# Kernel tuning notes

Measured on AMD Instinct MI355X. Metric: run time of the kernel, lower is better.

The kernel has to match this reference:

```python
import jax, jax.numpy as jnp
from jax import lax
import numpy as np

KSIZE = 3      # patch size for correlation
RATE = 2       # downsample rate; raw kernel = 2*RATE
FUSE_K = 3     # diagonal fuse kernel
SCALE = 10.0   # softmax_scale
DOWN_RATE = 8  # mask downsample
EPS = 1e-4
DN = ('NCHW', 'OIHW', 'NCHW')


def same_pad(x, k, s):
    H, W = x.shape[-2], x.shape[-1]
    oh, ow = -(-H // s), -(-W // s)
    ph = max(0, (oh - 1) * s + k - H)
    pw = max(0, (ow - 1) * s + k - W)
    pt, pl = ph // 2, pw // 2
    pad = [(0, 0)] * (x.ndim - 2) + [(pt, ph - pt), (pl, pw - pl)]
    return jnp.pad(x, pad)


def extract_patches(x, k, s):
    # x: [B,C,H,W] -> [B, L, C, k, k], matching torch unfold ordering
    B, C, H, W = x.shape
    oh, ow = -(-H // s), -(-W // s)
    xp = same_pad(x, k, s)
    cols = [xp[:, :, i:i + oh * s:s, j:j + ow * s:s] for i in range(k) for j in range(k)]
    p = jnp.stack(cols, axis=2).reshape(B, C, k, k, oh * ow)
    return p.transpose(0, 4, 1, 2, 3)


def conv1x1(x, w, b):  # x: [L,C,kh,kw], w: [D,C], b: [D]
    return jnp.einsum('lcij,dc->ldij', x, w) + b[None, :, None, None]


def setup_inputs():
    key = jax.random.key(0)
    B, C, H, W = 4, 128, 96, 96
    D = C // 8
    ks = jax.random.split(key, 6)
    f = jax.random.normal(ks[0], (B, C, H, W), jnp.float32)
    b = jax.random.normal(ks[1], (B, C, H, W), jnp.float32)
    mask = jnp.ones((B, 1, 4 * H, 4 * W), jnp.float32)
    mask = mask.at[:, :, 120:264, 120:264].set(0.0)  # rectangular hole
    s = 0.05
    wq = jax.random.normal(ks[2], (D, C), jnp.float32) * s
    bq = jnp.zeros((D,), jnp.float32)
    wk = jax.random.normal(ks[3], (D, C), jnp.float32) * s
    bk = jnp.zeros((D,), jnp.float32)
    wv = jax.random.normal(ks[4], (C, C), jnp.float32) * s
    bv = jnp.zeros((C,), jnp.float32)
    beta_2 = jnp.asarray(1.0, jnp.float32)
    return dict(f=f, b=b, mask=mask, wq=wq, bq=bq, wk=wk, bk=bk, wv=wv, bv=bv,
                beta_2=beta_2)


def reference(f, b, mask, wq, bq, wk, bk, wv, bv, beta_2):
    B, C, H, W = f.shape
    raw_w = extract_patches(b, 2 * RATE, RATE)          # [B, L, C, 4, 4]
    f_ds = f[:, :, ::RATE, ::RATE]                      # nearest 1/RATE
    b_ds = b[:, :, ::RATE, ::RATE]
    h, w_ = f_ds.shape[2], f_ds.shape[3]
    L = h * w_
    w_p = extract_patches(b_ds, KSIZE, 1)               # [B, L, C, 3, 3]
    fw_p = extract_patches(f_ds, KSIZE, 1)              # [B, L, C, 3, 3]
    m_ds = mask[:, :, ::DOWN_RATE, ::DOWN_RATE]
    m = extract_patches(m_ds, KSIZE, 1)[0]              # [L, 1, 3, 3] (batch 0, as in original)
    mm = lax.stop_gradient(
        (jnp.mean(m, axis=(1, 2, 3)) == 0.0).astype(f.dtype)).reshape(L, 1, 1)
    eye = jnp.eye(FUSE_K, dtype=f.dtype).reshape(1, 1, FUSE_K, FUSE_K)

    def one(fi_p, wi_p, xi, raw_wi):
        # intra-patch pixel attention (9x9 per patch)
        q = conv1x1(fi_p, wq, bq).reshape(L, -1, 9).transpose(0, 2, 1)   # [L,9,D]
        k_ = conv1x1(wi_p, wk, bk).reshape(L, -1, 9)                     # [L,D,9]
        sim = jnp.einsum('lnd,ldm->lnm', q, k_) * m.reshape(L, 1, 9)
        attn = jax.nn.softmax(sim, axis=-1)
        v = conv1x1(fi_p, wv, bv).reshape(L, C, 9)
        final = jnp.einsum('lcn,lmn->lcm', v, attn).reshape(L, C, KSIZE, KSIZE)
        final = beta_2 * fi_p * m + (1.0 - m) * final
        # normalize patch kernels
        norm = jnp.maximum(jnp.sqrt(jnp.sum(final * final, axis=(1, 2, 3), keepdims=True)), EPS)
        wn = final / norm                                                 # [L,C,3,3]
        # patch-correlation: conv with data-dependent kernels
        yi = lax.conv_general_dilated(same_pad(xi[None], KSIZE, 1), wn,
                                      (1, 1), 'VALID', dimension_numbers=DN)  # [1,L,h,w]
        # fuse: two diagonal-propagation convolutions
        y2 = yi.reshape(1, 1, L, L)
        y2 = lax.conv_general_dilated(y2, eye, (1, 1), ((1, 1), (1, 1)), dimension_numbers=DN)
        y2 = y2.reshape(h, w_, h, w_).transpose(1, 0, 3, 2).reshape(1, 1, L, L)
        y2 = lax.conv_general_dilated(y2, eye, (1, 1), ((1, 1), (1, 1)), dimension_numbers=DN)
        y2 = y2.reshape(w_, h, w_, h).transpose(1, 0, 3, 2)               # [h,w,h,w]
        yi = y2.reshape(L, h, w_) * mm
        yi = jax.nn.softmax(yi * SCALE, axis=0) * mm
        # conv_transpose2d(stride=RATE, padding=1) via lhs-dilated conv
        wt = jnp.flip(raw_wi, (-2, -1)).transpose(1, 0, 2, 3)             # [C,L,4,4]
        out = lax.conv_general_dilated(yi[None], wt, (1, 1), ((2, 2), (2, 2)),
                                       lhs_dilation=(RATE, RATE),
                                       dimension_numbers=DN) / 4.0
        return out[0]                                                     # [C,H,W]

    return jax.vmap(one)(fw_p, w_p, f_ds, raw_w)
```

## Files before the change

### kernel.cpp

```cpp
#include <hip/hip_runtime.h>
#include <math.h>


constexpr int B_ = 4, C_ = 128, D_ = 16;
constexpr int FH = 96, FW = 96;
constexpr int Hh = 48, Wd = 48;
constexpr int L_ = Hh * Wd;
constexpr int NEED_CAP = 384, HOLE_CAP = 320;
constexpr int KC = C_ * 9;
constexpr int QKV_ROWS = 208;
constexpr int NQK = NEED_CAP * 9;
constexpr float SCALE_ = 10.0f;
constexpr float EPS_ = 1e-4f;

typedef __attribute__((ext_vector_type(8))) short bf16x8;
typedef __attribute__((ext_vector_type(4))) float f32x4;
typedef __attribute__((ext_vector_type(4))) short s16x4;
typedef __attribute__((ext_vector_type(2))) unsigned short u16x2;

static __device__ __forceinline__ f32x4 mfma16(bf16x8 a, bf16x8 b, f32x4 c) {
  return __builtin_amdgcn_mfma_f32_16x16x32_bf16(a, b, c, 0, 0, 0);
}
static __device__ __forceinline__ unsigned short bf16_rne(float f) {
  unsigned u = __builtin_bit_cast(unsigned, f);
  unsigned r = (u + 0x7FFFu + ((u >> 16) & 1u)) >> 16;
  return (unsigned short)r;
}
static __device__ __forceinline__ float bf16f(unsigned short h) {
  unsigned u = ((unsigned)h) << 16;
  return __builtin_bit_cast(float, u);
}
static __device__ __forceinline__ void split2(float v, unsigned short& hi, unsigned short& lo) {
  hi = bf16_rne(v);
  lo = bf16_rne(v - bf16f(hi));
}

constexpr size_t A256(size_t v) { return (v + 255) & ~size_t(255); }
constexpr size_t OFF_META  = 0;
constexpr size_t OFF_MP    = A256(OFF_META + 64 * 4);
constexpr size_t OFF_MM    = A256(OFF_MP + (size_t)L_ * 9 * 4);
constexpr size_t OFF_ROWL  = A256(OFF_MM + (size_t)L_ * 4);
constexpr size_t OFF_NLIST = A256(OFF_ROWL + (size_t)L_ * 4);
constexpr size_t OFF_HLIST = A256(OFF_NLIST + (size_t)NEED_CAP * 4);
constexpr size_t OFF_WQVH  = A256(OFF_HLIST + (size_t)HOLE_CAP * 4);
constexpr size_t OFF_WQVL  = A256(OFF_WQVH + (size_t)192 * 128 * 2);
constexpr size_t OFF_WKH   = A256(OFF_WQVL + (size_t)192 * 128 * 2);
constexpr size_t OFF_WKL   = A256(OFF_WKH + (size_t)64 * 128 * 2);
constexpr size_t OFF_FDSH  = A256(OFF_WKL + (size_t)64 * 128 * 2);
constexpr size_t OFF_FDSL  = A256(OFF_FDSH + (size_t)B_ * L_ * C_ * 2);
constexpr size_t OFF_BDSH  = A256(OFF_FDSL + (size_t)B_ * L_ * C_ * 2);
constexpr size_t OFF_BDSL  = A256(OFF_BDSH + (size_t)B_ * L_ * C_ * 2);
constexpr size_t OFF_QKV   = A256(OFF_BDSL + (size_t)B_ * L_ * C_ * 2);
constexpr size_t OFF_SF    = OFF_QKV;
constexpr size_t OFF_WNH   = A256(OFF_QKV + (size_t)B_ * QKV_ROWS * NQK * 4);
constexpr size_t OFF_WNL   = A256(OFF_WNH + (size_t)B_ * NEED_CAP * KC * 2);
constexpr size_t OFF_SRAW  = A256(OFF_WNL + (size_t)B_ * NEED_CAP * KC * 2);
constexpr size_t OFF_PHT   = OFF_SRAW;
constexpr size_t OFF_PLT   = OFF_SRAW + (size_t)B_ * L_ * HOLE_CAP * 2;
constexpr size_t OFF_RW3H  = A256(OFF_SRAW + (size_t)B_ * NEED_CAP * L_ * 4);
constexpr size_t OFF_RW3L  = A256(OFF_RW3H + (size_t)B_ * 4 * C_ * 1280 * 2);
constexpr size_t OFF_OUTS  = A256(OFF_RW3L + (size_t)B_ * 4 * C_ * 1280 * 2);

__global__ __launch_bounds__(256) void gla_wpack(const float* __restrict__ wq, const float* __restrict__ wk,
                                                 const float* __restrict__ wv, char* __restrict__ ws)
{
  int i = blockIdx.x * 256 + threadIdx.x;
  unsigned short* qvh = (unsigned short*)(ws + OFF_WQVH);
  unsigned short* qvl = (unsigned short*)(ws + OFF_WQVL);
  unsigned short* kh  = (unsigned short*)(ws + OFF_WKH);
  unsigned short* kl  = (unsigned short*)(ws + OFF_WKL);
  if (i < 192 * 128) {
    int row = i >> 7, c = i & 127;
    float v = 0.f;
    if (row < 16) v = wq[row * C_ + c];
    else if (row < 144) v = wv[(row - 16) * C_ + c];
    unsigned short hi, lo; split2(v, hi, lo);
    qvh[i] = hi; qvl[i] = lo;
  } else if (i < 256 * 128) {
    int j = i - 192 * 128;
    int row = j >> 7, c = j & 127;
    float v = (row < 16) ? wk[row * C_ + c] : 0.f;
    unsigned short hi, lo; split2(v, hi, lo);
    kh[j] = hi; kl[j] = lo;
  }
}

__global__ __launch_bounds__(256) void gla_maskA(const float* __restrict__ mask, char* __restrict__ ws)
{
  int l = blockIdx.x * 256 + threadIdx.x;
  if (l >= L_) return;
  float* m_p = (float*)(ws + OFF_MP);
  int* mmi = (int*)(ws + OFF_MM);
  int y = l / Wd, x = l % Wd;
  bool all0 = true;
  #pragma unroll
  for (int dy = 0; dy < 3; dy++)
    #pragma unroll
    for (int dx = 0; dx < 3; dx++) {
      int sy = y + dy - 1, sx = x + dx - 1;
      float v = ((unsigned)sy < (unsigned)Hh && (unsigned)sx < (unsigned)Wd)
                ? mask[(size_t)(8 * sy) * 384 + 8 * sx] : 0.f;
      m_p[l * 9 + dy * 3 + dx] = v;
      if (v != 0.f) all0 = false;
    }
  mmi[l] = all0 ? 1 : 0;
}

__global__ __launch_bounds__(256) void gla_scan(char* __restrict__ ws)
{
  const int* mmi = (const int*)(ws + OFF_MM);
  int* row_l = (int*)(ws + OFF_ROWL);
  int* nlist = (int*)(ws + OFF_NLIST);
  int* hlist = (int*)(ws + OFF_HLIST);
  int* meta  = (int*)(ws + OFF_META);
  __shared__ int ns1[L_], nraw[L_];
  __shared__ int sN[256], sH[256];
  const int t = threadIdx.x;
  for (int l = t; l < L_; l += 256) { ns1[l] = 0; nraw[l] = 0; }
  __syncthreads();
  for (int l = t; l < L_; l += 256) {
    if (mmi[l]) {
      int i = l / Wd, j = l % Wd;
      int p2 = j * Hh + i;
      for (int k2 = -1; k2 <= 1; k2++) {
        int p2k = p2 + k2;
        if (p2k >= 0 && p2k < L_) {
          int j2 = p2k / Hh, i2 = p2k % Hh;
          ns1[i2 * Wd + j2] = 1;
        }
      }
    }
  }
  __syncthreads();
  for (int l = t; l < L_; l += 256) {
    if (ns1[l]) {
      for (int k1 = -1; k1 <= 1; k1++) {
        int l3 = l + k1;
        if (l3 >= 0 && l3 < L_) nraw[l3] = 1;
      }
    }
  }
  __syncthreads();
  int cN = 0, cH = 0;
  for (int q = 0; q < 9; q++) {
    int l = t * 9 + q;
    if (nraw[l]) cN++;
    if (mmi[l]) cH++;
  }
  sN[t] = cN; sH[t] = cH;
  __syncthreads();
  for (int off = 1; off < 256; off <<= 1) {
    int vN = (t >= off) ? sN[t - off] : 0;
    int vH = (t >= off) ? sH[t - off] : 0;
    __syncthreads();
    sN[t] += vN; sH[t] += vH;
    __syncthreads();
  }
  int bN = sN[t] - cN, bH = sH[t] - cH;
  for (int q = 0; q < 9; q++) {
    int l = t * 9 + q;
    int rl = -1;
    if (nraw[l]) { if (bN < NEED_CAP) { nlist[bN] = l; rl = bN; } bN++; }
    row_l[l] = rl;
    if (mmi[l]) { if (bH < HOLE_CAP) { hlist[bH] = l; } bH++; }
  }
  if (t == 255) {
    meta[0] = sN[255] < NEED_CAP ? sN[255] : NEED_CAP;
    meta[1] = sH[255] < HOLE_CAP ? sH[255] : HOLE_CAP;
  }
}

__global__ __launch_bounds__(256) void gla_splitfb(const float* __restrict__ f, const float* __restrict__ b,
                                                   char* __restrict__ ws)
{
  const int y = blockIdx.x, ib = blockIdx.y, z = blockIdx.z;
  const float* src = z ? b : f;
  unsigned short* dsth = (unsigned short*)(ws + (z ? OFF_BDSH : OFF_FDSH));
  unsigned short* dstl = (unsigned short*)(ws + (z ? OFF_BDSL : OFF_FDSL));
  __shared__ float tile[48][130];
  const int t = threadIdx.x;
  for (int idx = t; idx < 48 * C_; idx += 256) {
    int x = idx % 48, c = idx / 48;
    tile[x][c] = src[(((size_t)ib * C_ + c) * FH + 2 * y) * FW + 2 * x];
  }
  __syncthreads();
  for (int i = 0; i < 12; i++) {
    int p = t + i * 256;
    int c2 = p & 63, x = p >> 6;
    float v0 = tile[x][c2 * 2], v1 = tile[x][c2 * 2 + 1];
    unsigned short h0, l0, h1, l1;
    split2(v0, h0, l0);
    split2(v1, h1, l1);
    size_t o = ((size_t)ib * L_ + (size_t)y * Wd + x) * C_ + c2 * 2;
    *(u16x2*)&dsth[o] = u16x2{h0, h1};
    *(u16x2*)&dstl[o] = u16x2{l0, l1};
  }
}

__global__ __launch_bounds__(256) void gla_qkv(const float* __restrict__ bq, const float* __restrict__ bk,
                                               const float* __restrict__ bv, char* __restrict__ ws)
{
  const int* meta = (const int*)(ws + OFF_META);
  const int need = meta[0];
  int orig = blockIdx.x;
  int wg = (orig & 7) * 54 + (orig >> 3);
  bool isK = wg >= 324;
  int ib, mt, nt;
  if (!isK) { ib = wg / 81; int r2 = wg % 81; mt = r2 / 27; nt = r2 % 27; }
  else { int q2 = wg - 324; ib = q2 / 27; mt = 0; nt = q2 % 27; }
  const int m0 = mt * 64, n0 = nt * 128;
  const unsigned short* Ahg = (const unsigned short*)(ws + (isK ? OFF_WKH : OFF_WQVH));
  const unsigned short* Alg = (const unsigned short*)(ws + (isK ? OFF_WKL : OFF_WQVL));
  const unsigned short* Bhg = (const unsigned short*)(ws + (isK ? OFF_BDSH : OFF_FDSH)) + (size_t)ib * L_ * C_;
  const unsigned short* Blg = (const unsigned short*)(ws + (isK ? OFF_BDSL : OFF_FDSL)) + (size_t)ib * L_ * C_;
  const int* nlist = (const int*)(ws + OFF_NLIST);
  float* QKV = (float*)(ws + OFF_QKV) + (size_t)ib * QKV_ROWS * NQK;

  __shared__ short Ah[64][40], Al[64][40], Bh[128][40], Bl[128][40];
  const int tid = threadIdx.x;
  const int lane = tid & 63, w = tid >> 6;
  const int fr = lane & 15, kq = (lane >> 4) * 8;
  const int arow = tid & 63, aj = tid >> 6;
  const int bcol = tid & 127, bj = tid >> 7;

  const int col = n0 + bcol;
  const int r = col / 9, tap = col % 9;
  bool valid = (r < need);
  size_t bpos = 0;
  if (valid) {
    int l = nlist[r];
    int y = l / Wd, x = l % Wd;
    int sy = y + tap / 3 - 1, sx = x + tap % 3 - 1;
    valid = ((unsigned)sy < (unsigned)Hh) && ((unsigned)sx < (unsigned)Wd);
    if (valid) bpos = (size_t)(sy * Wd + sx) * C_;
  }

  f32x4 acc[4][2];
  #pragma unroll
  for (int mi = 0; mi < 4; mi++)
    #pragma unroll
    for (int ni = 0; ni < 2; ni++)
      #pragma unroll
      for (int q = 0; q < 4; q++) acc[mi][ni][q] = 0.f;

  const bf16x8 zz = {0, 0, 0, 0, 0, 0, 0, 0};
  bf16x8 rah, ral, rbh0, rbh1, rbl0, rbl1;
  auto load_step = [&](int s) {
    int k0 = s * 32;
    size_t aoff = (size_t)(m0 + arow) * 128 + k0 + aj * 8;
    rah = *(const bf16x8*)&Ahg[aoff];
    ral = *(const bf16x8*)&Alg[aoff];
    if (valid) {
      size_t boff = bpos + k0 + bj * 16;
      rbh0 = *(const bf16x8*)&Bhg[boff];
      rbh1 = *(const bf16x8*)&Bhg[boff + 8];
      rbl0 = *(const bf16x8*)&Blg[boff];
      rbl1 = *(const bf16x8*)&Blg[boff + 8];
    } else {
      rbh0 = zz; rbh1 = zz; rbl0 = zz; rbl1 = zz;
    }
  };

  load_step(0);
  for (int s = 0; s < 4; s++) {
    __syncthreads();
    *(bf16x8*)&Ah[arow][aj * 8] = rah;
    *(bf16x8*)&Al[arow][aj * 8] = ral;
    *(bf16x8*)&Bh[bcol][bj * 16] = rbh0;
    *(bf16x8*)&Bh[bcol][bj * 16 + 8] = rbh1;
    *(bf16x8*)&Bl[bcol][bj * 16] = rbl0;
    *(bf16x8*)&Bl[bcol][bj * 16 + 8] = rbl1;
    __syncthreads();
    if (s < 3) load_step(s + 1);
    bf16x8 a_h[4], a_l[4], b_h[2], b_l[2];
    #pragma unroll
    for (int mi = 0; mi < 4; mi++) {
      a_h[mi] = *(const bf16x8*)&Ah[mi * 16 + fr][kq];
      a_l[mi] = *(const bf16x8*)&Al[mi * 16 + fr][kq];
    }
    #pragma unroll
    for (int ni = 0; ni < 2; ni++) {
      b_h[ni] = *(const bf16x8*)&Bh[w * 32 + ni * 16 + fr][kq];
      b_l[ni] = *(const bf16x8*)&Bl[w * 32 + ni * 16 + fr][kq];
    }
    #pragma unroll
    for (int mi = 0; mi < 4; mi++)
      #pragma unroll
      for (int ni = 0; ni < 2; ni++) {
        acc[mi][ni] = mfma16(a_h[mi], b_h[ni], acc[mi][ni]);
        acc[mi][ni] = mfma16(a_h[mi], b_l[ni], acc[mi][ni]);
        acc[mi][ni] = mfma16(a_l[mi], b_h[ni], acc[mi][ni]);
      }
  }
  #pragma unroll
  for (int mi = 0; mi < 4; mi++)
    #pragma unroll
    for (int ni = 0; ni < 2; ni++) {
      int rowb = m0 + mi * 16 + (lane >> 4) * 4;
      int colg = n0 + w * 32 + ni * 16 + fr;
      #pragma unroll
      for (int q = 0; q < 4; q++) {
        int row = rowb + q;
        float v = acc[mi][ni][q];
        if (!isK) {
          float bias = row < 16 ? bq[row] : (row < 144 ? bv[row - 16] : 0.f);
          QKV[(size_t)row * NQK + colg] = v + bias;
        } else if (row < 16) {
          QKV[(size_t)(192 + row) * NQK + colg] = v + bk[row];
        }
      }
    }
}

__global__ __launch_bounds__(128) void gla_patch2(const float* __restrict__ beta2p, char* __restrict__ ws)
{
  const int* meta = (const int*)(ws + OFF_META);
  int r = blockIdx.x;
  if (r >= meta[0]) return;
  int ib = blockIdx.y;
  const int* nlist = (const int*)(ws + OFF_NLIST);
  const float* m_p = (const float*)(ws + OFF_MP);
  const float* QKV = (const float*)(ws + OFF_QKV) + (size_t)ib * QKV_ROWS * NQK;
  const unsigned short* fdsh = (const unsigned short*)(ws + OFF_FDSH) + (size_t)ib * L_ * C_;
  const unsigned short* fdsl = (const unsigned short*)(ws + OFF_FDSL) + (size_t)ib * L_ * C_;
  unsigned short* wnh = (unsigned short*)(ws + OFF_WNH) + ((size_t)ib * NEED_CAP + r) * KC;
  unsigned short* wnl = (unsigned short*)(ws + OFF_WNL) + ((size_t)ib * NEED_CAP + r) * KC;

  __shared__ float qs[144], ks[144], att[81], mps[9], red[128];
  const int t = threadIdx.x;
  const int l = nlist[r];
  const int y = l / Wd, x = l % Wd;
  const int colb = r * 9;

  if (t < 9) mps[t] = m_p[l * 9 + t];
  for (int o = t; o < 288; o += 128) {
    if (o < 144) {
      int n = o / 16, d = o % 16;
      qs[o] = QKV[(size_t)d * NQK + colb + n];
    } else {
      int o2 = o - 144;
      int d = o2 / 9, m = o2 % 9;
      ks[o2] = QKV[(size_t)(192 + d) * NQK + colb + m];
    }
  }
  __syncthreads();
  if (t < 81) {
    int n = t / 9, m = t % 9;
    float s = 0.f;
    #pragma unroll
    for (int d = 0; d < 16; d++) s += qs[n * 16 + d] * ks[d * 9 + m];
    att[t] = s * mps[m];
  }
  __syncthreads();
  if (t < 9) {
    float mx = -1e30f;
    for (int m = 0; m < 9; m++) mx = fmaxf(mx, att[t * 9 + m]);
    float e[9], sm = 0.f;
    for (int m = 0; m < 9; m++) { e[m] = expf(att[t * 9 + m] - mx); sm += e[m]; }
    float inv = 1.f / sm;
    for (int m = 0; m < 9; m++) att[t * 9 + m] = e[m] * inv;
  }
  __syncthreads();
  const int c = t;
  float vn[9], fi[9];
  #pragma unroll
  for (int n = 0; n < 9; n++) vn[n] = QKV[(size_t)(16 + c) * NQK + colb + n];
  #pragma unroll
  for (int m = 0; m < 9; m++) {
    int sy = y + m / 3 - 1, sx = x + m % 3 - 1;
    float v = 0.f;
    if ((unsigned)sy < (unsigned)Hh && (unsigned)sx < (unsigned)Wd) {
      size_t o = (size_t)(sy * Wd + sx) * C_ + c;
      v = bf16f(fdsh[o]) + bf16f(fdsl[o]);
    }
    fi[m] = v;
  }
  float beta2 = beta2p[0];
  float fm[9];
  #pragma unroll
  for (int m = 0; m < 9; m++) {
    float s = 0.f;
    #pragma unroll
    for (int n = 0; n < 9; n++) s += vn[n] * att[m * 9 + n];
    float mp = mps[m];
    fm[m] = beta2 * fi[m] * mp + (1.f - mp) * s;
  }
  float ss = 0.f;
  #pragma unroll
  for (int m = 0; m < 9; m++) ss += fm[m] * fm[m];
  red[t] = ss;
  __syncthreads();
  for (int off = 64; off > 0; off >>= 1) {
    if (t < off) red[t] += red[t + off];
    __syncthreads();
  }
  float inv = 1.f / fmaxf(sqrtf(red[0]), EPS_);
  #pragma unroll
  for (int m = 0; m < 9; m++) {
    unsigned short hi, lo;
    split2(fm[m] * inv, hi, lo);
    wnh[m * C_ + c] = hi;
    wnl[m * C_ + c] = lo;
  }
}

__global__ __launch_bounds__(256) void gla_corr(char* __restrict__ ws)
{
  int orig = blockIdx.x;
  int wg = (orig & 7) * 54 + (orig >> 3);
  int xt = wg % 18;
  int rt = (wg / 18) % 6;
  int ib = wg / 108;
  const int r0 = rt * 64, x0 = xt * 128;

  const unsigned short* Ahg = (const unsigned short*)(ws + OFF_WNH) + (size_t)ib * NEED_CAP * KC;
  const unsigned short* Alg = (const unsigned short*)(ws + OFF_WNL) + (size_t)ib * NEED_CAP * KC;
  const unsigned short* fh = (const unsigned short*)(ws + OFF_FDSH) + (size_t)ib * L_ * C_;
  const unsigned short* fl = (const unsigned short*)(ws + OFF_FDSL) + (size_t)ib * L_ * C_;
  float* S = (float*)(ws + OFF_SRAW) + (size_t)ib * NEED_CAP * L_;

  __shared__ short Ah[64][40], Al[64][40], Bh[128][40], Bl[128][40];
  const int tid = threadIdx.x;
  const int lane = tid & 63, w = tid >> 6;
  const int fr = lane & 15, kq = (lane >> 4) * 8;
  const int arow = tid & 63, aj = tid >> 6;
  const int bcol = tid & 127, bj = tid >> 7;
  const int xg = x0 + bcol;
  const int aa = xg / Wd, bb = xg % Wd;

  f32x4 acc[4][2];
  #pragma unroll
  for (int mi = 0; mi < 4; mi++)
    #pragma unroll
    for (int ni = 0; ni < 2; ni++)
      #pragma unroll
      for (int q = 0; q < 4; q++) acc[mi][ni][q] = 0.f;

  const bf16x8 zz = {0, 0, 0, 0, 0, 0, 0, 0};
  bf16x8 rah, ral, rbh0, rbh1, rbl0, rbl1;

  auto load_step = [&](int s) {
    int tap = s >> 2, kc = s & 3;
    size_t aoff = (size_t)(r0 + arow) * KC + tap * 128 + kc * 32 + aj * 8;
    rah = *(const bf16x8*)&Ahg[aoff];
    ral = *(const bf16x8*)&Alg[aoff];
    int dyv = tap / 3, dxv = tap - 3 * dyv;
    int sy = aa + dyv - 1, sx = bb + dxv - 1;
    if (((unsigned)sy < (unsigned)Hh) & ((unsigned)sx < (unsigned)Wd)) {
      size_t bpos = (size_t)(sy * Wd + sx) * C_ + kc * 32 + bj * 16;
      rbh0 = *(const bf16x8*)&fh[bpos];
      rbh1 = *(const bf16x8*)&fh[bpos + 8];
      rbl0 = *(const bf16x8*)&fl[bpos];
      rbl1 = *(const bf16x8*)&fl[bpos + 8];
    } else {
      rbh0 = zz; rbh1 = zz; rbl0 = zz; rbl1 = zz;
    }
  };

  load_step(0);
  for (int s = 0; s < 36; s++) {
    __syncthreads();
    *(bf16x8*)&Ah[arow][aj * 8] = rah;
    *(bf16x8*)&Al[arow][aj * 8] = ral;
    *(bf16x8*)&Bh[bcol][bj * 16] = rbh0;
    *(bf16x8*)&Bh[bcol][bj * 16 + 8] = rbh1;
    *(bf16x8*)&Bl[bcol][bj * 16] = rbl0;
    *(bf16x8*)&Bl[bcol][bj * 16 + 8] = rbl1;
    __syncthreads();
    if (s < 35) load_step(s + 1);
    bf16x8 a_h[4], a_l[4], b_h[2], b_l[2];
    #pragma unroll
    for (int mi = 0; mi < 4; mi++) {
      a_h[mi] = *(const bf16x8*)&Ah[mi * 16 + fr][kq];
      a_l[mi] = *(const bf16x8*)&Al[mi * 16 + fr][kq];
    }
    #pragma unroll
    for (int ni = 0; ni < 2; ni++) {
      b_h[ni] = *(const bf16x8*)&Bh[w * 32 + ni * 16 + fr][kq];
      b_l[ni] = *(const bf16x8*)&Bl[w * 32 + ni * 16 + fr][kq];
    }
    #pragma unroll
    for (int mi = 0; mi < 4; mi++)
      #pragma unroll
      for (int ni = 0; ni < 2; ni++) {
        acc[mi][ni] = mfma16(a_h[mi], b_h[ni], acc[mi][ni]);
        acc[mi][ni] = mfma16(a_h[mi], b_l[ni], acc[mi][ni]);
        acc[mi][ni] = mfma16(a_l[mi], b_h[ni], acc[mi][ni]);
      }
  }
  #pragma unroll
  for (int mi = 0; mi < 4; mi++)
    #pragma unroll
    for (int ni = 0; ni < 2; ni++) {
      int row0 = r0 + mi * 16 + (lane >> 4) * 4;
      int col = x0 + w * 32 + ni * 16 + fr;
      #pragma unroll
      for (int q = 0; q < 4; q++)
        S[(size_t)(row0 + q) * L_ + col] = acc[mi][ni][q];
    }
}

__global__ __launch_bounds__(256) void gla_fuse(char* __restrict__ ws)
{
  const int* meta = (const int*)(ws + OFF_META);
  int rh = blockIdx.y;
  if (rh >= meta[1]) return;
  int ib = blockIdx.z;
  const int* hlist = (const int*)(ws + OFF_HLIST);
  const int* row_l = (const int*)(ws + OFF_ROWL);
  const float* S = (const float*)(ws + OFF_SRAW) + (size_t)ib * NEED_CAP * L_;
  float* Sf = (float*)(ws + OFF_SF) + ((size_t)ib * HOLE_CAP + rh) * L_;
  int x = blockIdx.x * 256 + threadIdx.x;
  int l = hlist[rh];
  int i = l / Wd, j = l % Wd;
  int a = x / Wd, b = x % Wd;
  int p2 = j * Hh + i, q2 = b * Hh + a;
  float acc = 0.f;
  #pragma unroll
  for (int k2 = -1; k2 <= 1; k2++) {
    int p2k = p2 + k2, q2k = q2 + k2;
    if (p2k < 0 || p2k >= L_ || q2k < 0 || q2k >= L_) continue;
    int j2 = p2k / Hh, i2 = p2k % Hh;
    int b2 = q2k / Hh, a2 = q2k % Hh;
    int l1 = i2 * Wd + j2, x1 = a2 * Wd + b2;
    #pragma unroll
    for (int k1 = -1; k1 <= 1; k1++) {
      int l3 = l1 + k1, x3 = x1 + k1;
      if (l3 < 0 || l3 >= L_ || x3 < 0 || x3 >= L_) continue;
      int r = row_l[l3];
      if (r >= 0) acc += S[(size_t)r * L_ + x3];
    }
  }
  Sf[x] = acc;
}

__global__ __launch_bounds__(256) void gla_softmax(char* __restrict__ ws)
{
  const int* meta = (const int*)(ws + OFF_META);
  const int hc = meta[1];
  const int ib = blockIdx.y;
  const int t = threadIdx.x;
  const int xl = t & 63, g = t >> 6;
  const int x0 = blockIdx.x * 64;
  const float* Sf = (const float*)(ws + OFF_SF) + (size_t)ib * HOLE_CAP * L_;
  unsigned short* Ph = (unsigned short*)(ws + OFF_PHT) + (size_t)ib * L_ * HOLE_CAP;
  unsigned short* Pl = (unsigned short*)(ws + OFF_PLT) + (size_t)ib * L_ * HOLE_CAP;
  __shared__ float red[4][64];
  __shared__ float smx[64], sinv[64];
  __shared__ short Th[64][72], Tl[64][72];
  const int x = x0 + xl;
  float mx = 0.f;
  for (int rh = g; rh < hc; rh += 4) mx = fmaxf(mx, SCALE_ * Sf[(size_t)rh * L_ + x]);
  red[g][xl] = mx;
  __syncthreads();
  mx = fmaxf(fmaxf(red[0][xl], red[1][xl]), fmaxf(red[2][xl], red[3][xl]));
  __syncthreads();
  float s = 0.f;
  for (int rh = g; rh < hc; rh += 4) s += expf(SCALE_ * Sf[(size_t)rh * L_ + x] - mx);
  red[g][xl] = s;
  __syncthreads();
  float den = (float)(L_ - hc) * expf(-mx) + red[0][xl] + red[1][xl] + red[2][xl] + red[3][xl];
  if (g == 0) { smx[xl] = mx; sinv[xl] = 1.f / den; }
  __syncthreads();
  for (int rh0 = 0; rh0 < HOLE_CAP; rh0 += 64) {
    for (int i = 0; i < 16; i++) {
      int idx = t + i * 256;
      int xl2 = idx & 63, rr = idx >> 6;
      int rh = rh0 + rr;
      float e = 0.f;
      if (rh < hc) e = expf(SCALE_ * Sf[(size_t)rh * L_ + x0 + xl2] - smx[xl2]) * sinv[xl2];
      unsigned short hi, lo;
      split2(e, hi, lo);
      Th[xl2][rr] = (short)hi;
      Tl[xl2][rr] = (short)lo;
    }
    __syncthreads();
    for (int i = 0; i < 4; i++) {
      int q = t + i * 256;
      int rq = q & 15, xl2 = q >> 4;
      size_t dst = (size_t)(x0 + xl2) * HOLE_CAP + rh0 + rq * 4;
      *(s16x4*)&Ph[dst] = *(const s16x4*)&Th[xl2][rq * 4];
      *(s16x4*)&Pl[dst] = *(const s16x4*)&Tl[xl2][rq * 4];
    }
    __syncthreads();
  }
}

__global__ __launch_bounds__(256) void gla_packRW3(const float* __restrict__ b, char* __restrict__ ws)
{
  int idx = blockIdx.x * 256 + threadIdx.x;
  const int tot = B_ * 4 * C_ * 1280;
  if (idx >= tot) return;
  const int* meta = (const int*)(ws + OFF_META);
  const int* hlist = (const int*)(ws + OFF_HLIST);
  unsigned short* RH = (unsigned short*)(ws + OFF_RW3H);
  unsigned short* RL = (unsigned short*)(ws + OFF_RW3L);
  int kk = idx % 1280;
  int c = (idx / 1280) & 127;
  int par = (idx / (1280 * 128)) & 3;
  int ib = idx / (1280 * 128 * 4);
  int tap = kk / 320, rh = kk % 320;
  int dy = tap >> 1, dx = tap & 1;
  int pY = par >> 1, pX = par & 1;
  float v = 0.f;
  if (rh < meta[1]) {
    int l = hlist[rh];
    int yy = l / Wd, xx = l % Wd;
    int ty = 2 * dy + ((pY + 1) & 1);
    int tx = 2 * dx + ((pX + 1) & 1);
    int sy = 2 * yy - 1 + ty, sx = 2 * xx - 1 + tx;
    if ((unsigned)sy < (unsigned)FH && (unsigned)sx < (unsigned)FW)
      v = b[(((size_t)ib * C_ + c) * FH + sy) * FW + sx];
  }
  unsigned short hi, lo;
  split2(v, hi, lo);
  RH[idx] = hi;
  RL[idx] = lo;
}

__global__ __launch_bounds__(256) void gla_out(char* __restrict__ ws)
{
  const int* meta = (const int*)(ws + OFF_META);
  const int rsteps = (meta[1] + 31) >> 5;
  const int nsteps = 4 * rsteps;
  int orig = blockIdx.x;
  int wg = (orig & 7) * 144 + (orig >> 3);
  int nt = wg % 36;
  int rest = wg / 36;
  int mt = rest & 1;
  int par = (rest >> 1) & 3;
  int ib = rest >> 3;
  const int m0 = mt * 64, n0 = nt * 64;
  const int pY = par >> 1, pX = par & 1;

  const unsigned short* Ahg = (const unsigned short*)(ws + OFF_RW3H) + ((size_t)(ib * 4 + par) * C_) * 1280;
  const unsigned short* Alg = (const unsigned short*)(ws + OFF_RW3L) + ((size_t)(ib * 4 + par) * C_) * 1280;
  const unsigned short* Ph = (const unsigned short*)(ws + OFF_PHT) + (size_t)ib * L_ * HOLE_CAP;
  const unsigned short* Pl = (const unsigned short*)(ws + OFF_PLT) + (size_t)ib * L_ * HOLE_CAP;
  float* OUTS = (float*)(ws + OFF_OUTS) + (size_t)(ib * 4 + par) * C_ * L_;

  __shared__ short Ah[64][40], Al[64][40], Bh[64][40], Bl[64][40];
  const int tid = threadIdx.x;
  const int lane = tid & 63, w = tid >> 6;
  const int fr = lane & 15, kq = (lane >> 4) * 8;
  const int arow = tid & 63, aj = tid >> 6;
  const int bcol = tid & 63, bj = tid >> 6;

  const int colg = n0 + bcol;
  const int Yh = colg / 48, Xh = colg % 48;
  size_t bpos[4];
  bool bval[4];
  #pragma unroll
  for (int j = 0; j < 4; j++) {
    int dy = j >> 1, dx = j & 1;
    int ay = Yh + pY - dy, bx = Xh + pX - dx;
    bval[j] = ((unsigned)ay < 48u) && ((unsigned)bx < 48u);
    bpos[j] = bval[j] ? (size_t)(ay * 48 + bx) * HOLE_CAP : 0;
  }

  f32x4 acc[4];
  #pragma unroll
  for (int mi = 0; mi < 4; mi++)
    #pragma unroll
    for (int q = 0; q < 4; q++) acc[mi][q] = 0.f;

  const bf16x8 zz = {0, 0, 0, 0, 0, 0, 0, 0};
  bf16x8 rah, ral, rbh, rbl;
  auto load_step = [&](int s) {
    int tap = s / rsteps;
    int kr = (s - tap * rsteps) * 32;
    size_t aoff = (size_t)(m0 + arow) * 1280 + tap * 320 + kr + aj * 8;
    rah = *(const bf16x8*)&Ahg[aoff];
    ral = *(const bf16x8*)&Alg[aoff];
    if (bval[tap]) {
      size_t boff = bpos[tap] + kr + bj * 8;
      rbh = *(const bf16x8*)&Ph[boff];
      rbl = *(const bf16x8*)&Pl[boff];
    } else {
      rbh = zz; rbl = zz;
    }
  };

  load_step(0);
  for (int s = 0; s < nsteps; s++) {
    __syncthreads();
    *(bf16x8*)&Ah[arow][aj * 8] = rah;
    *(bf16x8*)&Al[arow][aj * 8] = ral;
    *(bf16x8*)&Bh[bcol][bj * 8] = rbh;
    *(bf16x8*)&Bl[bcol][bj * 8] = rbl;
    __syncthreads();
    if (s + 1 < nsteps) load_step(s + 1);
    bf16x8 b_h = *(const bf16x8*)&Bh[w * 16 + fr][kq];
    bf16x8 b_l = *(const bf16x8*)&Bl[w * 16 + fr][kq];
    #pragma unroll
    for (int mi = 0; mi < 4; mi++) {
      bf16x8 a_h = *(const bf16x8*)&Ah[mi * 16 + fr][kq];
      bf16x8 a_l = *(const bf16x8*)&Al[mi * 16 + fr][kq];
      acc[mi] = mfma16(a_h, b_h, acc[mi]);
      acc[mi] = mfma16(a_h, b_l, acc[mi]);
      acc[mi] = mfma16(a_l, b_h, acc[mi]);
    }
  }
  #pragma unroll
  for (int mi = 0; mi < 4; mi++) {
    int c0 = m0 + mi * 16 + (lane >> 4) * 4;
    int colpos = n0 + w * 16 + fr;
    #pragma unroll
    for (int q = 0; q < 4; q++)
      OUTS[(size_t)(c0 + q) * L_ + colpos] = 0.25f * acc[mi][q];
  }
}

__global__ __launch_bounds__(256) void gla_inter(float* __restrict__ out, const char* __restrict__ ws)
{
  int idx = blockIdx.x * 256 + threadIdx.x;
  if (idx >= B_ * C_ * FH * (FW / 2)) return;
  const float* OUTS = (const float*)(ws + OFF_OUTS);
  int Xh = idx % 48;
  int Y  = (idx / 48) % FH;
  int c  = (idx / (48 * FH)) % C_;
  int ib = idx / (48 * FH * C_);
  int pY = Y & 1, Yh = Y >> 1;
  size_t base = ((size_t)(ib * 4 + pY * 2) * C_ + c) * L_ + Yh * 48 + Xh;
  float2 o2;
  o2.x = OUTS[base];
  o2.y = OUTS[base + (size_t)C_ * L_];
  *(float2*)&out[(((size_t)ib * C_ + c) * FH + Y) * FW + 2 * Xh] = o2;
}

extern "C" void kernel_launch(void* const* d_in, const int* in_sizes, int n_in,
                              void* d_out, int out_size, void* d_ws, size_t ws_size,
                              hipStream_t stream)
{
  (void)in_sizes; (void)n_in; (void)out_size; (void)ws_size;
  const float* f    = (const float*)d_in[0];
  const float* b    = (const float*)d_in[1];
  const float* mask = (const float*)d_in[2];
  const float* wq   = (const float*)d_in[3];
  const float* bq   = (const float*)d_in[4];
  const float* wk   = (const float*)d_in[5];
  const float* bk   = (const float*)d_in[6];
  const float* wv   = (const float*)d_in[7];
  const float* bv   = (const float*)d_in[8];
  const float* bt2  = (const float*)d_in[9];
  float* out = (float*)d_out;
  char* ws = (char*)d_ws;

  hipLaunchKernelGGL(gla_wpack, dim3(128), dim3(256), 0, stream, wq, wk, wv, ws);
  hipLaunchKernelGGL(gla_maskA, dim3(9), dim3(256), 0, stream, mask, ws);
  hipLaunchKernelGGL(gla_scan, dim3(1), dim3(256), 0, stream, ws);
  hipLaunchKernelGGL(gla_splitfb, dim3(Hh, B_, 2), dim3(256), 0, stream, f, b, ws);
  hipLaunchKernelGGL(gla_qkv, dim3(432), dim3(256), 0, stream, bq, bk, bv, ws);
  hipLaunchKernelGGL(gla_patch2, dim3(NEED_CAP, B_), dim3(128), 0, stream, bt2, ws);
  hipLaunchKernelGGL(gla_corr, dim3(432), dim3(256), 0, stream, ws);
  hipLaunchKernelGGL(gla_fuse, dim3(L_ / 256, HOLE_CAP, B_), dim3(256), 0, stream, ws);
  hipLaunchKernelGGL(gla_softmax, dim3(L_ / 64, B_), dim3(256), 0, stream, ws);
  hipLaunchKernelGGL(gla_packRW3, dim3((B_ * 4 * C_ * 1280 + 255) / 256), dim3(256), 0, stream, b, ws);
  hipLaunchKernelGGL(gla_out, dim3(1152), dim3(256), 0, stream, ws);
  hipLaunchKernelGGL(gla_inter, dim3((B_ * C_ * FH * (FW / 2) + 255) / 256), dim3(256), 0, stream, out, ws);
}
```

Measured before the change: 351.7 us.

## Double-buffer LDS in corr/out GEMMs, widen out tile, swizzle fuse grid

```diff
diff --git a/kernel.cpp b/kernel.cpp
--- a/kernel.cpp
+++ b/kernel.cpp
@@ -419,7 +419,7 @@
   const unsigned short* fl = (const unsigned short*)(ws + OFF_FDSL) + (size_t)ib * L_ * C_;
   float* S = (float*)(ws + OFF_SRAW) + (size_t)ib * NEED_CAP * L_;
 
-  __shared__ short Ah[64][40], Al[64][40], Bh[128][40], Bl[128][40];
+  __shared__ short Ah[2][64][40], Al[2][64][40], Bh[2][128][40], Bl[2][128][40];
   const int tid = threadIdx.x;
   const int lane = tid & 63, w = tid >> 6;
   const int fr = lane & 15, kq = (lane >> 4) * 8;
@@ -437,9 +437,11 @@
       for (int q = 0; q < 4; q++) acc[mi][ni][q] = 0.f;
 
   const bf16x8 zz = {0, 0, 0, 0, 0, 0, 0, 0};
-  bf16x8 rah, ral, rbh0, rbh1, rbl0, rbl1;
-
-  auto load_step = [&](int s) {
+  bf16x8 rahA, ralA, rb0A, rb1A, rb2A, rb3A;
+  bf16x8 rahB, ralB, rb0B, rb1B, rb2B, rb3B;
+
+  auto load_step = [&](int s, bf16x8& rah, bf16x8& ral, bf16x8& rbh0, bf16x8& rbh1,
+                       bf16x8& rbl0, bf16x8& rbl1) {
     int tap = s >> 2, kc = s & 3;
     size_t aoff = (size_t)(r0 + arow) * KC + tap * 128 + kc * 32 + aj * 8;
     rah = *(const bf16x8*)&Ahg[aoff];
@@ -456,28 +458,26 @@
       rbh0 = zz; rbh1 = zz; rbl0 = zz; rbl1 = zz;
     }
   };
-
-  load_step(0);
-  for (int s = 0; s < 36; s++) {
-    __syncthreads();
-    *(bf16x8*)&Ah[arow][aj * 8] = rah;
-    *(bf16x8*)&Al[arow][aj * 8] = ral;
-    *(bf16x8*)&Bh[bcol][bj * 16] = rbh0;
-    *(bf16x8*)&Bh[bcol][bj * 16 + 8] = rbh1;
-    *(bf16x8*)&Bl[bcol][bj * 16] = rbl0;
-    *(bf16x8*)&Bl[bcol][bj * 16 + 8] = rbl1;
-    __syncthreads();
-    if (s < 35) load_step(s + 1);
+  auto store_step = [&](int bi, bf16x8 rah, bf16x8 ral, bf16x8 rbh0, bf16x8 rbh1,
+                        bf16x8 rbl0, bf16x8 rbl1) {
+    *(bf16x8*)&Ah[bi][arow][aj * 8] = rah;
+    *(bf16x8*)&Al[bi][arow][aj * 8] = ral;
+    *(bf16x8*)&Bh[bi][bcol][bj * 16] = rbh0;
+    *(bf16x8*)&Bh[bi][bcol][bj * 16 + 8] = rbh1;
+    *(bf16x8*)&Bl[bi][bcol][bj * 16] = rbl0;
+    *(bf16x8*)&Bl[bi][bcol][bj * 16 + 8] = rbl1;
+  };
+  auto compute = [&](int bi) {
     bf16x8 a_h[4], a_l[4], b_h[2], b_l[2];
     #pragma unroll
     for (int mi = 0; mi < 4; mi++) {
-      a_h[mi] = *(const bf16x8*)&Ah[mi * 16 + fr][kq];
-      a_l[mi] = *(const bf16x8*)&Al[mi * 16 + fr][kq];
+      a_h[mi] = *(const bf16x8*)&Ah[bi][mi * 16 + fr][kq];
+      a_l[mi] = *(const bf16x8*)&Al[bi][mi * 16 + fr][kq];
     }
     #pragma unroll
     for (int ni = 0; ni < 2; ni++) {
-      b_h[ni] = *(const bf16x8*)&Bh[w * 32 + ni * 16 + fr][kq];
-      b_l[ni] = *(const bf16x8*)&Bl[w * 32 + ni * 16 + fr][kq];
+      b_h[ni] = *(const bf16x8*)&Bh[bi][w * 32 + ni * 16 + fr][kq];
+      b_l[ni] = *(const bf16x8*)&Bl[bi][w * 32 + ni * 16 + fr][kq];
     }
     #pragma unroll
     for (int mi = 0; mi < 4; mi++)
@@ -487,6 +487,24 @@
         acc[mi][ni] = mfma16(a_h[mi], b_l[ni], acc[mi][ni]);
         acc[mi][ni] = mfma16(a_l[mi], b_h[ni], acc[mi][ni]);
       }
+  };
+
+  const int nsteps = 36;
+  load_step(0, rahA, ralA, rb0A, rb1A, rb2A, rb3A);
+  load_step(1, rahB, ralB, rb0B, rb1B, rb2B, rb3B);
+  store_step(0, rahA, ralA, rb0A, rb1A, rb2A, rb3A);
+  __syncthreads();
+  for (int s = 0; s < nsteps; s += 2) {
+    compute(0);
+    if (s + 2 < nsteps) load_step(s + 2, rahA, ralA, rb0A, rb1A, rb2A, rb3A);
+    store_step(1, rahB, ralB, rb0B, rb1B, rb2B, rb3B);
+    __syncthreads();
+    compute(1);
+    if (s + 3 < nsteps) load_step(s + 3, rahB, ralB, rb0B, rb1B, rb2B, rb3B);
+    if (s + 2 < nsteps) {
+      store_step(0, rahA, ralA, rb0A, rb1A, rb2A, rb3A);
+      __syncthreads();
+    }
   }
   #pragma unroll
   for (int mi = 0; mi < 4; mi++)
@@ -503,14 +521,17 @@
 __global__ __launch_bounds__(256) void gla_fuse(char* __restrict__ ws)
 {
   const int* meta = (const int*)(ws + OFF_META);
-  int rh = blockIdx.y;
+  int orig = blockIdx.x;
+  int wg = (orig & 7) * 1440 + (orig >> 3);
+  int xc = wg % 9;
+  int rh = (wg / 9) % HOLE_CAP;
+  int ib = wg / (9 * HOLE_CAP);
   if (rh >= meta[1]) return;
-  int ib = blockIdx.z;
   const int* hlist = (const int*)(ws + OFF_HLIST);
   const int* row_l = (const int*)(ws + OFF_ROWL);
   const float* S = (const float*)(ws + OFF_SRAW) + (size_t)ib * NEED_CAP * L_;
   float* Sf = (float*)(ws + OFF_SF) + ((size_t)ib * HOLE_CAP + rh) * L_;
-  int x = blockIdx.x * 256 + threadIdx.x;
+  int x = xc * 256 + threadIdx.x;
   int l = hlist[rh];
   int i = l / Wd, j = l % Wd;
   int a = x / Wd, b = x % Wd;
@@ -624,13 +645,12 @@
   const int rsteps = (meta[1] + 31) >> 5;
   const int nsteps = 4 * rsteps;
   int orig = blockIdx.x;
-  int wg = (orig & 7) * 144 + (orig >> 3);
-  int nt = wg % 36;
-  int rest = wg / 36;
-  int mt = rest & 1;
-  int par = (rest >> 1) & 3;
-  int ib = rest >> 3;
-  const int m0 = mt * 64, n0 = nt * 64;
+  int wg = (orig & 7) * 72 + (orig >> 3);
+  int nt = wg % 18;
+  int mt = (wg / 18) % 2;
+  int par = (wg / 36) % 4;
+  int ib = wg / 144;
+  const int m0 = mt * 64, n0 = nt * 128;
   const int pY = par >> 1, pX = par & 1;
 
   const unsigned short* Ahg = (const unsigned short*)(ws + OFF_RW3H) + ((size_t)(ib * 4 + par) * C_) * 1280;
@@ -639,76 +659,104 @@
   const unsigned short* Pl = (const unsigned short*)(ws + OFF_PLT) + (size_t)ib * L_ * HOLE_CAP;
   float* OUTS = (float*)(ws + OFF_OUTS) + (size_t)(ib * 4 + par) * C_ * L_;
 
-  __shared__ short Ah[64][40], Al[64][40], Bh[64][40], Bl[64][40];
+  __shared__ short Ah[2][64][40], Al[2][64][40], Bh[2][128][40], Bl[2][128][40];
   const int tid = threadIdx.x;
   const int lane = tid & 63, w = tid >> 6;
   const int fr = lane & 15, kq = (lane >> 4) * 8;
   const int arow = tid & 63, aj = tid >> 6;
-  const int bcol = tid & 63, bj = tid >> 6;
+  const int bcol = tid & 127, bj = tid >> 7;
 
   const int colg = n0 + bcol;
   const int Yh = colg / 48, Xh = colg % 48;
-  size_t bpos[4];
-  bool bval[4];
-  #pragma unroll
-  for (int j = 0; j < 4; j++) {
-    int dy = j >> 1, dx = j & 1;
-    int ay = Yh + pY - dy, bx = Xh + pX - dx;
-    bval[j] = ((unsigned)ay < 48u) && ((unsigned)bx < 48u);
-    bpos[j] = bval[j] ? (size_t)(ay * 48 + bx) * HOLE_CAP : 0;
-  }
-
-  f32x4 acc[4];
+
+  f32x4 acc[4][2];
   #pragma unroll
   for (int mi = 0; mi < 4; mi++)
     #pragma unroll
-    for (int q = 0; q < 4; q++) acc[mi][q] = 0.f;
+    for (int ni = 0; ni < 2; ni++)
+      #pragma unroll
+      for (int q = 0; q < 4; q++) acc[mi][ni][q] = 0.f;
 
   const bf16x8 zz = {0, 0, 0, 0, 0, 0, 0, 0};
-  bf16x8 rah, ral, rbh, rbl;
-  auto load_step = [&](int s) {
+  bf16x8 rahA, ralA, rb0A, rb1A, rb2A, rb3A;
+  bf16x8 rahB, ralB, rb0B, rb1B, rb2B, rb3B;
+
+  auto load_step = [&](int s, bf16x8& rah, bf16x8& ral, bf16x8& rbh0, bf16x8& rbh1,
+                       bf16x8& rbl0, bf16x8& rbl1) {
     int tap = s / rsteps;
     int kr = (s - tap * rsteps) * 32;
     size_t aoff = (size_t)(m0 + arow) * 1280 + tap * 320 + kr + aj * 8;
     rah = *(const bf16x8*)&Ahg[aoff];
     ral = *(const bf16x8*)&Alg[aoff];
-    if (bval[tap]) {
-      size_t boff = bpos[tap] + kr + bj * 8;
-      rbh = *(const bf16x8*)&Ph[boff];
-      rbl = *(const bf16x8*)&Pl[boff];
+    int ay = Yh + pY - (tap >> 1);
+    int bx = Xh + pX - (tap & 1);
+    if (((unsigned)ay < 48u) & ((unsigned)bx < 48u)) {
+      size_t boff = (size_t)(ay * 48 + bx) * HOLE_CAP + kr + bj * 16;
+      rbh0 = *(const bf16x8*)&Ph[boff];
+      rbh1 = *(const bf16x8*)&Ph[boff + 8];
+      rbl0 = *(const bf16x8*)&Pl[boff];
+      rbl1 = *(const bf16x8*)&Pl[boff + 8];
     } else {
-      rbh = zz; rbl = zz;
+      rbh0 = zz; rbh1 = zz; rbl0 = zz; rbl1 = zz;
     }
   };
-
-  load_step(0);
-  for (int s = 0; s < nsteps; s++) {
+  auto store_step = [&](int bi, bf16x8 rah, bf16x8 ral, bf16x8 rbh0, bf16x8 rbh1,
+                        bf16x8 rbl0, bf16x8 rbl1) {
+    *(bf16x8*)&Ah[bi][arow][aj * 8] = rah;
+    *(bf16x8*)&Al[bi][arow][aj * 8] = ral;
+    *(bf16x8*)&Bh[bi][bcol][bj * 16] = rbh0;
+    *(bf16x8*)&Bh[bi][bcol][bj * 16 + 8] = rbh1;
+    *(bf16x8*)&Bl[bi][bcol][bj * 16] = rbl0;
+    *(bf16x8*)&Bl[bi][bcol][bj * 16 + 8] = rbl1;
+  };
+  auto compute = [&](int bi) {
+    bf16x8 a_h[4], a_l[4], b_h[2], b_l[2];
+    #pragma unroll
+    for (int mi = 0; mi < 4; mi++) {
+      a_h[mi] = *(const bf16x8*)&Ah[bi][mi * 16 + fr][kq];
+      a_l[mi] = *(const bf16x8*)&Al[bi][mi * 16 + fr][kq];
+    }
+    #pragma unroll
+    for (int ni = 0; ni < 2; ni++) {
+      b_h[ni] = *(const bf16x8*)&Bh[bi][w * 32 + ni * 16 + fr][kq];
+      b_l[ni] = *(const bf16x8*)&Bl[bi][w * 32 + ni * 16 + fr][kq];
+    }
+    #pragma unroll
+    for (int mi = 0; mi < 4; mi++)
+      #pragma unroll
+      for (int ni = 0; ni < 2; ni++) {
+        acc[mi][ni] = mfma16(a_h[mi], b_h[ni], acc[mi][ni]);
+        acc[mi][ni] = mfma16(a_h[mi], b_l[ni], acc[mi][ni]);
+        acc[mi][ni] = mfma16(a_l[mi], b_h[ni], acc[mi][ni]);
+      }
+  };
+
+  load_step(0, rahA, ralA, rb0A, rb1A, rb2A, rb3A);
+  load_step(1, rahB, ralB, rb0B, rb1B, rb2B, rb3B);
+  store_step(0, rahA, ralA, rb0A, rb1A, rb2A, rb3A);
+  __syncthreads();
+  for (int s = 0; s < nsteps; s += 2) {
+    compute(0);
+    if (s + 2 < nsteps) load_step(s + 2, rahA, ralA, rb0A, rb1A, rb2A, rb3A);
+    store_step(1, rahB, ralB, rb0B, rb1B, rb2B, rb3B);
     __syncthreads();
-    *(bf16x8*)&Ah[arow][aj * 8] = rah;
-    *(bf16x8*)&Al[arow][aj * 8] = ral;
-    *(bf16x8*)&Bh[bcol][bj * 8] = rbh;
-    *(bf16x8*)&Bl[bcol][bj * 8] = rbl;
-    __syncthreads();
-    if (s + 1 < nsteps) load_step(s + 1);
-    bf16x8 b_h = *(const bf16x8*)&Bh[w * 16 + fr][kq];
-    bf16x8 b_l = *(const bf16x8*)&Bl[w * 16 + fr][kq];
-    #pragma unroll
-    for (int mi = 0; mi < 4; mi++) {
-      bf16x8 a_h = *(const bf16x8*)&Ah[mi * 16 + fr][kq];
-      bf16x8 a_l = *(const bf16x8*)&Al[mi * 16 + fr][kq];
-      acc[mi] = mfma16(a_h, b_h, acc[mi]);
-      acc[mi] = mfma16(a_h, b_l, acc[mi]);
-      acc[mi] = mfma16(a_l, b_h, acc[mi]);
-    }
-  }
-  #pragma unroll
-  for (int mi = 0; mi < 4; mi++) {
-    int c0 = m0 + mi * 16 + (lane >> 4) * 4;
-    int colpos = n0 + w * 16 + fr;
-    #pragma unroll
-    for (int q = 0; q < 4; q++)
-      OUTS[(size_t)(c0 + q) * L_ + colpos] = 0.25f * acc[mi][q];
-  }
+    compute(1);
+    if (s + 3 < nsteps) load_step(s + 3, rahB, ralB, rb0B, rb1B, rb2B, rb3B);
+    if (s + 2 < nsteps) {
+      store_step(0, rahA, ralA, rb0A, rb1A, rb2A, rb3A);
+      __syncthreads();
+    }
+  }
+  #pragma unroll
+  for (int mi = 0; mi < 4; mi++)
+    #pragma unroll
+    for (int ni = 0; ni < 2; ni++) {
+      int c0 = m0 + mi * 16 + (lane >> 4) * 4;
+      int colpos = n0 + w * 32 + ni * 16 + fr;
+      #pragma unroll
+      for (int q = 0; q < 4; q++)
+        OUTS[(size_t)(c0 + q) * L_ + colpos] = 0.25f * acc[mi][ni][q];
+    }
 }
 
 __global__ __launch_bounds__(256) void gla_inter(float* __restrict__ out, const char* __restrict__ ws)
@@ -753,9 +801,9 @@
   hipLaunchKernelGGL(gla_qkv, dim3(432), dim3(256), 0, stream, bq, bk, bv, ws);
   hipLaunchKernelGGL(gla_patch2, dim3(NEED_CAP, B_), dim3(128), 0, stream, bt2, ws);
   hipLaunchKernelGGL(gla_corr, dim3(432), dim3(256), 0, stream, ws);
-  hipLaunchKernelGGL(gla_fuse, dim3(L_ / 256, HOLE_CAP, B_), dim3(256), 0, stream, ws);
+  hipLaunchKernelGGL(gla_fuse, dim3(9 * HOLE_CAP * B_), dim3(256), 0, stream, ws);
   hipLaunchKernelGGL(gla_softmax, dim3(L_ / 64, B_), dim3(256), 0, stream, ws);
   hipLaunchKernelGGL(gla_packRW3, dim3((B_ * 4 * C_ * 1280 + 255) / 256), dim3(256), 0, stream, b, ws);
-  hipLaunchKernelGGL(gla_out, dim3(1152), dim3(256), 0, stream, ws);
+  hipLaunchKernelGGL(gla_out, dim3(576), dim3(256), 0, stream, ws);
   hipLaunchKernelGGL(gla_inter, dim3((B_ * C_ * FH * (FW / 2) + 255) / 256), dim3(256), 0, stream, out, ws);
 }
```

After: 364.0 us. 1.03x slower.

## Split-K the correlation and output GEMMs into two halves with partial buffers

Applied to the files above, without the earlier changes.

```diff
diff --git a/kernel.cpp b/kernel.cpp
--- a/kernel.cpp
+++ b/kernel.cpp
@@ -52,12 +52,14 @@
 constexpr size_t OFF_BDSL  = A256(OFF_BDSH + (size_t)B_ * L_ * C_ * 2);
 constexpr size_t OFF_QKV   = A256(OFF_BDSL + (size_t)B_ * L_ * C_ * 2);
 constexpr size_t OFF_SF    = OFF_QKV;
+constexpr size_t OFF_OUTSB = OFF_FDSH;
 constexpr size_t OFF_WNH   = A256(OFF_QKV + (size_t)B_ * QKV_ROWS * NQK * 4);
 constexpr size_t OFF_WNL   = A256(OFF_WNH + (size_t)B_ * NEED_CAP * KC * 2);
 constexpr size_t OFF_SRAW  = A256(OFF_WNL + (size_t)B_ * NEED_CAP * KC * 2);
 constexpr size_t OFF_PHT   = OFF_SRAW;
 constexpr size_t OFF_PLT   = OFF_SRAW + (size_t)B_ * L_ * HOLE_CAP * 2;
 constexpr size_t OFF_RW3H  = A256(OFF_SRAW + (size_t)B_ * NEED_CAP * L_ * 4);
+constexpr size_t OFF_SRAW2 = OFF_RW3H;
 constexpr size_t OFF_RW3L  = A256(OFF_RW3H + (size_t)B_ * 4 * C_ * 1280 * 2);
 constexpr size_t OFF_OUTS  = A256(OFF_RW3L + (size_t)B_ * 4 * C_ * 1280 * 2);
 
@@ -407,17 +409,20 @@
 __global__ __launch_bounds__(256) void gla_corr(char* __restrict__ ws)
 {
   int orig = blockIdx.x;
-  int wg = (orig & 7) * 54 + (orig >> 3);
+  int wg = (orig & 7) * 108 + (orig >> 3);
   int xt = wg % 18;
   int rt = (wg / 18) % 6;
-  int ib = wg / 108;
+  int rest = wg / 108;
+  int h = rest & 1;
+  int ib = rest >> 1;
   const int r0 = rt * 64, x0 = xt * 128;
+  const int s_begin = h * 18, s_end = s_begin + 18;
 
   const unsigned short* Ahg = (const unsigned short*)(ws + OFF_WNH) + (size_t)ib * NEED_CAP * KC;
   const unsigned short* Alg = (const unsigned short*)(ws + OFF_WNL) + (size_t)ib * NEED_CAP * KC;
   const unsigned short* fh = (const unsigned short*)(ws + OFF_FDSH) + (size_t)ib * L_ * C_;
   const unsigned short* fl = (const unsigned short*)(ws + OFF_FDSL) + (size_t)ib * L_ * C_;
-  float* S = (float*)(ws + OFF_SRAW) + (size_t)ib * NEED_CAP * L_;
+  float* S = (float*)(ws + (h ? OFF_SRAW2 : OFF_SRAW)) + (size_t)ib * NEED_CAP * L_;
 
   __shared__ short Ah[64][40], Al[64][40], Bh[128][40], Bl[128][40];
   const int tid = threadIdx.x;
@@ -457,8 +462,8 @@
     }
   };
 
-  load_step(0);
-  for (int s = 0; s < 36; s++) {
+  load_step(s_begin);
+  for (int s = s_begin; s < s_end; s++) {
     __syncthreads();
     *(bf16x8*)&Ah[arow][aj * 8] = rah;
     *(bf16x8*)&Al[arow][aj * 8] = ral;
@@ -467,7 +472,7 @@
     *(bf16x8*)&Bl[bcol][bj * 16] = rbl0;
     *(bf16x8*)&Bl[bcol][bj * 16 + 8] = rbl1;
     __syncthreads();
-    if (s < 35) load_step(s + 1);
+    if (s + 1 < s_end) load_step(s + 1);
     bf16x8 a_h[4], a_l[4], b_h[2], b_l[2];
     #pragma unroll
     for (int mi = 0; mi < 4; mi++) {
@@ -503,14 +508,18 @@
 __global__ __launch_bounds__(256) void gla_fuse(char* __restrict__ ws)
 {
   const int* meta = (const int*)(ws + OFF_META);
-  int rh = blockIdx.y;
+  int orig = blockIdx.x;
+  int wg = (orig & 7) * 1440 + (orig >> 3);
+  int xc = wg % 9;
+  int rh = (wg / 9) % HOLE_CAP;
+  int ib = wg / (9 * HOLE_CAP);
   if (rh >= meta[1]) return;
-  int ib = blockIdx.z;
   const int* hlist = (const int*)(ws + OFF_HLIST);
   const int* row_l = (const int*)(ws + OFF_ROWL);
-  const float* S = (const float*)(ws + OFF_SRAW) + (size_t)ib * NEED_CAP * L_;
+  const float* S1 = (const float*)(ws + OFF_SRAW) + (size_t)ib * NEED_CAP * L_;
+  const float* S2 = (const float*)(ws + OFF_SRAW2) + (size_t)ib * NEED_CAP * L_;
   float* Sf = (float*)(ws + OFF_SF) + ((size_t)ib * HOLE_CAP + rh) * L_;
-  int x = blockIdx.x * 256 + threadIdx.x;
+  int x = xc * 256 + threadIdx.x;
   int l = hlist[rh];
   int i = l / Wd, j = l % Wd;
   int a = x / Wd, b = x % Wd;
@@ -528,7 +537,10 @@
       int l3 = l1 + k1, x3 = x1 + k1;
       if (l3 < 0 || l3 >= L_ || x3 < 0 || x3 >= L_) continue;
       int r = row_l[l3];
-      if (r >= 0) acc += S[(size_t)r * L_ + x3];
+      if (r >= 0) {
+        size_t o = (size_t)r * L_ + x3;
+        acc += S1[o] + S2[o];
+      }
     }
   }
   Sf[x] = acc;
@@ -622,22 +634,24 @@
 {
   const int* meta = (const int*)(ws + OFF_META);
   const int rsteps = (meta[1] + 31) >> 5;
-  const int nsteps = 4 * rsteps;
   int orig = blockIdx.x;
-  int wg = (orig & 7) * 144 + (orig >> 3);
+  int wg = (orig & 7) * 288 + (orig >> 3);
   int nt = wg % 36;
   int rest = wg / 36;
   int mt = rest & 1;
   int par = (rest >> 1) & 3;
-  int ib = rest >> 3;
+  int ibh = rest >> 3;
+  int ib = ibh >> 1;
+  int h = ibh & 1;
   const int m0 = mt * 64, n0 = nt * 64;
   const int pY = par >> 1, pX = par & 1;
+  const int s_begin = 2 * h * rsteps, s_end = s_begin + 2 * rsteps;
 
   const unsigned short* Ahg = (const unsigned short*)(ws + OFF_RW3H) + ((size_t)(ib * 4 + par) * C_) * 1280;
   const unsigned short* Alg = (const unsigned short*)(ws + OFF_RW3L) + ((size_t)(ib * 4 + par) * C_) * 1280;
   const unsigned short* Ph = (const unsigned short*)(ws + OFF_PHT) + (size_t)ib * L_ * HOLE_CAP;
   const unsigned short* Pl = (const unsigned short*)(ws + OFF_PLT) + (size_t)ib * L_ * HOLE_CAP;
-  float* OUTS = (float*)(ws + OFF_OUTS) + (size_t)(ib * 4 + par) * C_ * L_;
+  float* OUTS = (float*)(ws + (h ? OFF_OUTSB : OFF_OUTS)) + (size_t)(ib * 4 + par) * C_ * L_;
 
   __shared__ short Ah[64][40], Al[64][40], Bh[64][40], Bl[64][40];
   const int tid = threadIdx.x;
@@ -648,15 +662,6 @@
 
   const int colg = n0 + bcol;
   const int Yh = colg / 48, Xh = colg % 48;
-  size_t bpos[4];
-  bool bval[4];
-  #pragma unroll
-  for (int j = 0; j < 4; j++) {
-    int dy = j >> 1, dx = j & 1;
-    int ay = Yh + pY - dy, bx = Xh + pX - dx;
-    bval[j] = ((unsigned)ay < 48u) && ((unsigned)bx < 48u);
-    bpos[j] = bval[j] ? (size_t)(ay * 48 + bx) * HOLE_CAP : 0;
-  }
 
   f32x4 acc[4];
   #pragma unroll
@@ -672,8 +677,10 @@
     size_t aoff = (size_t)(m0 + arow) * 1280 + tap * 320 + kr + aj * 8;
     rah = *(const bf16x8*)&Ahg[aoff];
     ral = *(const bf16x8*)&Alg[aoff];
-    if (bval[tap]) {
-      size_t boff = bpos[tap] + kr + bj * 8;
+    int ay = Yh + pY - (tap >> 1);
+    int bx = Xh + pX - (tap & 1);
+    if (((unsigned)ay < 48u) & ((unsigned)bx < 48u)) {
+      size_t boff = (size_t)(ay * 48 + bx) * HOLE_CAP + kr + bj * 8;
       rbh = *(const bf16x8*)&Ph[boff];
       rbl = *(const bf16x8*)&Pl[boff];
     } else {
@@ -681,15 +688,15 @@
     }
   };
 
-  load_step(0);
-  for (int s = 0; s < nsteps; s++) {
+  load_step(s_begin);
+  for (int s = s_begin; s < s_end; s++) {
     __syncthreads();
     *(bf16x8*)&Ah[arow][aj * 8] = rah;
     *(bf16x8*)&Al[arow][aj * 8] = ral;
     *(bf16x8*)&Bh[bcol][bj * 8] = rbh;
     *(bf16x8*)&Bl[bcol][bj * 8] = rbl;
     __syncthreads();
-    if (s + 1 < nsteps) load_step(s + 1);
+    if (s + 1 < s_end) load_step(s + 1);
     bf16x8 b_h = *(const bf16x8*)&Bh[w * 16 + fr][kq];
     bf16x8 b_l = *(const bf16x8*)&Bl[w * 16 + fr][kq];
     #pragma unroll
@@ -716,15 +723,17 @@
   int idx = blockIdx.x * 256 + threadIdx.x;
   if (idx >= B_ * C_ * FH * (FW / 2)) return;
   const float* OUTS = (const float*)(ws + OFF_OUTS);
+  const float* OUTSB = (const float*)(ws + OFF_OUTSB);
   int Xh = idx % 48;
   int Y  = (idx / 48) % FH;
   int c  = (idx / (48 * FH)) % C_;
   int ib = idx / (48 * FH * C_);
   int pY = Y & 1, Yh = Y >> 1;
   size_t base = ((size_t)(ib * 4 + pY * 2) * C_ + c) * L_ + Yh * 48 + Xh;
+  size_t base2 = base + (size_t)C_ * L_;
   float2 o2;
-  o2.x = OUTS[base];
-  o2.y = OUTS[base + (size_t)C_ * L_];
+  o2.x = OUTS[base] + OUTSB[base];
+  o2.y = OUTS[base2] + OUTSB[base2];
   *(float2*)&out[(((size_t)ib * C_ + c) * FH + Y) * FW + 2 * Xh] = o2;
 }
 
@@ -752,10 +761,10 @@
   hipLaunchKernelGGL(gla_splitfb, dim3(Hh, B_, 2), dim3(256), 0, stream, f, b, ws);
   hipLaunchKernelGGL(gla_qkv, dim3(432), dim3(256), 0, stream, bq, bk, bv, ws);
   hipLaunchKernelGGL(gla_patch2, dim3(NEED_CAP, B_), dim3(128), 0, stream, bt2, ws);
-  hipLaunchKernelGGL(gla_corr, dim3(432), dim3(256), 0, stream, ws);
-  hipLaunchKernelGGL(gla_fuse, dim3(L_ / 256, HOLE_CAP, B_), dim3(256), 0, stream, ws);
+  hipLaunchKernelGGL(gla_corr, dim3(864), dim3(256), 0, stream, ws);
+  hipLaunchKernelGGL(gla_fuse, dim3(9 * HOLE_CAP * B_), dim3(256), 0, stream, ws);
   hipLaunchKernelGGL(gla_softmax, dim3(L_ / 64, B_), dim3(256), 0, stream, ws);
   hipLaunchKernelGGL(gla_packRW3, dim3((B_ * 4 * C_ * 1280 + 255) / 256), dim3(256), 0, stream, b, ws);
-  hipLaunchKernelGGL(gla_out, dim3(1152), dim3(256), 0, stream, ws);
+  hipLaunchKernelGGL(gla_out, dim3(2304), dim3(256), 0, stream, ws);
   hipLaunchKernelGGL(gla_inter, dim3((B_ * C_ * FH * (FW / 2) + 255) / 256), dim3(256), 0, stream, out, ws);
 }
```

New measurement: 356.0 us. No clear change (+1.2%).
